# Performance work log

Measured on AMD Instinct MI355X. Metric: run time of the kernel, lower is better.

Reference implementation:

```python
import jax, jax.numpy as jnp
import numpy as np

EPS = 1e-6
DN = ('NCHW', 'OIHW', 'NCHW')


def _dw_conv(s, w, dilation, k):
    pad = dilation * (k - 1) // 2
    return jax.lax.conv_general_dilated(
        s, w, window_strides=(1, 1), padding=[(pad, pad), (pad, pad)],
        rhs_dilation=(dilation, dilation), dimension_numbers=DN,
        feature_group_count=4)


def _branch(s, dw_w, pw_w, pw_b, dilation, k):
    h = _dw_conv(s, dw_w, dilation, k)           # [B,4,H,W]
    # pointwise 1x1 conv 4 -> 1
    return jnp.einsum('bchw,oc->bohw', h, pw_w) + pw_b[None, :, None, None]


def setup_inputs() -> dict:
    key = jax.random.key(0)
    ks = jax.random.split(key, 12)
    B, C, H, W = 32, 64, 128, 128
    nb, rh = 3, 8
    d = {}
    d['x'] = jax.random.normal(ks[0], (B, C, H, W), dtype=jnp.float32)
    # branch 0: k=3 d=1; branch 1: k=7 d=1; branch 2: k=7 d=2
    d['dw0'] = jax.random.normal(ks[1], (4, 1, 3, 3), dtype=jnp.float32) * 0.2
    d['dw1'] = jax.random.normal(ks[2], (4, 1, 7, 7), dtype=jnp.float32) * 0.1
    d['dw2'] = jax.random.normal(ks[3], (4, 1, 7, 7), dtype=jnp.float32) * 0.1
    d['pw0_w'] = jax.random.normal(ks[4], (1, 4), dtype=jnp.float32) * 0.5
    d['pw0_b'] = jnp.zeros((1,), dtype=jnp.float32)
    d['pw1_w'] = jax.random.normal(ks[5], (1, 4), dtype=jnp.float32) * 0.5
    d['pw1_b'] = jnp.zeros((1,), dtype=jnp.float32)
    d['pw2_w'] = jax.random.normal(ks[6], (1, 4), dtype=jnp.float32) * 0.5
    d['pw2_b'] = jnp.zeros((1,), dtype=jnp.float32)
    # router: 1x1 convs on pooled [B,4,1,1] == dense layers
    d['rw1'] = jax.random.normal(ks[7], (rh, 4), dtype=jnp.float32) * 0.5
    d['rb1'] = jnp.zeros((rh,), dtype=jnp.float32)
    d['rw2'] = jax.random.normal(ks[8], (nb, rh), dtype=jnp.float32) * 0.3
    d['rb2'] = jnp.zeros((nb,), dtype=jnp.float32)
    # t_raw = softplus_inverse(1.0)
    d['t_raw'] = jnp.asarray(np.log(np.expm1(1.0)), dtype=jnp.float32)
    return d


def reference(x, dw0, dw1, dw2, pw0_w, pw0_b, pw1_w, pw1_b, pw2_w, pw2_b,
              rw1, rb1, rw2, rb2, t_raw):
    B, C, H, W = x.shape
    avg_map = jnp.mean(x, axis=1, keepdims=True)        # [B,1,H,W]
    max_map = jnp.max(x, axis=1, keepdims=True)         # [B,1,H,W]
    xs = jnp.linspace(-1.0, 1.0, W, dtype=x.dtype)
    ys = jnp.linspace(-1.0, 1.0, H, dtype=x.dtype)
    yy, xx = jnp.meshgrid(ys, xs, indexing='ij')
    xg = jnp.broadcast_to(xx[None, None], (B, 1, H, W))
    yg = jnp.broadcast_to(yy[None, None], (B, 1, H, W))
    s = jnp.concatenate([avg_map, max_map, xg, yg], axis=1)  # [B,4,H,W]

    # router: global avg pool -> 1x1 conv -> relu -> 1x1 conv -> softmax
    pooled = jnp.mean(s, axis=(2, 3))                    # [B,4]
    hid = jax.nn.relu(pooled @ rw1.T + rb1)              # [B,rh]
    logits = hid @ rw2.T + rb2                           # [B,nb]
    rw = jax.nn.softmax(logits, axis=1)                  # [B,nb]

    z = jnp.stack([
        _branch(s, dw0, pw0_w, pw0_b, 1, 3),
        _branch(s, dw1, pw1_w, pw1_b, 1, 7),
        _branch(s, dw2, pw2_w, pw2_b, 2, 7),
    ], axis=1)                                           # [B,nb,1,H,W]

    wlogits = jnp.sum(rw[:, :, None, None, None] * z, axis=1)  # [B,1,H,W]
    T = jax.nn.softplus(t_raw) + EPS
    sa = jax.nn.sigmoid(wlogits / T)                     # [B,1,H,W]
    Y = x * sa                                           # [B,C,H,W]
    return (Y, sa)
```

## Files before the change

kernel.cpp:

```cpp
#include <hip/hip_runtime.h>

#define B_ 32
#define C_ 64
#define H_ 128
#define W_ 128
#define HW_ (H_*W_)
#define CHW_ (C_*HW_)

__global__ __launch_bounds__(256) void k1_reduce(
    const float* __restrict__ x, float* __restrict__ avgmap,
    float* __restrict__ maxmap, float* __restrict__ partial)
{
    int t = blockIdx.x * 256 + threadIdx.x;
    int base = t * 4;
    int b = base >> 14;
    int q = base & (HW_ - 1);
    const float4* xp = (const float4*)(x + (size_t)b * CHW_ + q);
    float4 v = xp[0];
    float4 s = v, m = v;
    #pragma unroll 8
    for (int c = 1; c < C_; ++c) {
        float4 u = xp[c * (HW_ / 4)];
        s.x += u.x; s.y += u.y; s.z += u.z; s.w += u.w;
        m.x = fmaxf(m.x, u.x); m.y = fmaxf(m.y, u.y);
        m.z = fmaxf(m.z, u.z); m.w = fmaxf(m.w, u.w);
    }
    const float inv = 1.0f / C_;
    float4 a = make_float4(s.x * inv, s.y * inv, s.z * inv, s.w * inv);
    ((float4*)avgmap)[t] = a;
    ((float4*)maxmap)[t] = m;

    float la = a.x + a.y + a.z + a.w;
    float lm = m.x + m.y + m.z + m.w;
    #pragma unroll
    for (int o = 32; o > 0; o >>= 1) {
        la += __shfl_down(la, o);
        lm += __shfl_down(lm, o);
    }
    __shared__ float wa[4], wm[4];
    int lane = threadIdx.x & 63, wid = threadIdx.x >> 6;
    if (lane == 0) { wa[wid] = la; wm[wid] = lm; }
    __syncthreads();
    if (threadIdx.x == 0) {
        partial[2 * blockIdx.x]     = wa[0] + wa[1] + wa[2] + wa[3];
        partial[2 * blockIdx.x + 1] = wm[0] + wm[1] + wm[2] + wm[3];
    }
}

__global__ void k2_router(const float* __restrict__ partial,
                          const float* __restrict__ rw1, const float* __restrict__ rb1,
                          const float* __restrict__ rw2, const float* __restrict__ rb2,
                          float* __restrict__ rwout)
{
    int b = threadIdx.x;
    if (b >= B_) return;
    float s0 = 0.0f, s1 = 0.0f;
    #pragma unroll
    for (int i = 0; i < 16; ++i) {
        s0 += partial[2 * (b * 16 + i)];
        s1 += partial[2 * (b * 16 + i) + 1];
    }
    float p0 = s0 * (1.0f / HW_);
    float p1 = s1 * (1.0f / HW_);
    float hid[8];
    #pragma unroll
    for (int j = 0; j < 8; ++j)
        hid[j] = fmaxf(0.0f, rb1[j] + rw1[j * 4] * p0 + rw1[j * 4 + 1] * p1);
    float lg[3];
    #pragma unroll
    for (int i = 0; i < 3; ++i) {
        float acc = rb2[i];
        #pragma unroll
        for (int j = 0; j < 8; ++j) acc += hid[j] * rw2[i * 8 + j];
        lg[i] = acc;
    }
    float mx = fmaxf(lg[0], fmaxf(lg[1], lg[2]));
    float e0 = expf(lg[0] - mx), e1 = expf(lg[1] - mx), e2 = expf(lg[2] - mx);
    float inv = 1.0f / (e0 + e1 + e2);
    rwout[b * 3 + 0] = e0 * inv;
    rwout[b * 3 + 1] = e1 * inv;
    rwout[b * 3 + 2] = e2 * inv;
}

__global__ __launch_bounds__(256) void k34_branches_apply(
    const float* __restrict__ x,
    const float* __restrict__ avgmap, const float* __restrict__ maxmap,
    const float* __restrict__ dw0, const float* __restrict__ dw1,
    const float* __restrict__ dw2,
    const float* __restrict__ pw0w, const float* __restrict__ pw0b,
    const float* __restrict__ pw1w, const float* __restrict__ pw1b,
    const float* __restrict__ pw2w, const float* __restrict__ pw2b,
    const float* __restrict__ rw, const float* __restrict__ t_raw,
    float* __restrict__ y, float* __restrict__ sa_out)
{
    __shared__ float sA[14][140];
    __shared__ float sM[14][140];
    __shared__ float wf0[36], wf1[196], wf2[196];
    __shared__ float ssa[256];

    int b  = blockIdx.y;
    int y0 = blockIdx.x * 2;
    int tix = threadIdx.x;
    const float* am = avgmap + (size_t)b * HW_;
    const float* mm = maxmap + (size_t)b * HW_;

    for (int idx = tix; idx < 14 * 32; idx += 256) {
        int r = idx >> 5, c4 = idx & 31;
        int gy = y0 - 6 + r;
        bool ok = (unsigned)gy < H_;
        float4 av = ok ? ((const float4*)(am + gy * W_))[c4]
                       : make_float4(0.f, 0.f, 0.f, 0.f);
        float4 mv = ok ? ((const float4*)(mm + gy * W_))[c4]
                       : make_float4(0.f, 0.f, 0.f, 0.f);
        float* pa = &sA[r][6 + c4 * 4];
        float* pm = &sM[r][6 + c4 * 4];
        pa[0] = av.x; pa[1] = av.y; pa[2] = av.z; pa[3] = av.w;
        pm[0] = mv.x; pm[1] = mv.y; pm[2] = mv.z; pm[3] = mv.w;
    }
    for (int idx = tix; idx < 14 * 12; idx += 256) {
        int r = idx / 12, c = idx % 12;
        int cc = (c < 6) ? c : (134 + c - 6);
        sA[r][cc] = 0.0f;
        sM[r][cc] = 0.0f;
    }
    if (tix < 36)  wf0[tix] = pw0w[tix / 9]  * dw0[tix];
    if (tix < 196) {
        wf1[tix] = pw1w[tix / 49] * dw1[tix];
        wf2[tix] = pw2w[tix / 49] * dw2[tix];
    }
    __syncthreads();

    int ly = tix >> 7;
    int lx = tix & 127;
    int gy = y0 + ly;
    const float sc = 2.0f / 127.0f;
    const float xv_c = lx * sc - 1.0f;

    float z0 = pw0b[0], z1 = pw1b[0], z2 = pw2b[0];

    #pragma unroll
    for (int ky = 0; ky < 3; ++ky) {
        #pragma unroll
        for (int kx = 0; kx < 3; ++kx) {
            int i = ky - 1, j = kx - 1;
            float a = sA[ly + 6 + i][lx + 6 + j];
            float m = sM[ly + 6 + i][lx + 6 + j];
            int iy = gy + i, ix = lx + j;
            bool ok = ((unsigned)iy < H_) && ((unsigned)ix < W_);
            float xv = ok ? (ix * sc - 1.0f) : 0.0f;
            float yv = ok ? (iy * sc - 1.0f) : 0.0f;
            int t = ky * 3 + kx;
            z0 += wf0[t] * a + wf0[9 + t] * m + wf0[18 + t] * xv + wf0[27 + t] * yv;
        }
    }
    #pragma unroll
    for (int ky = 0; ky < 7; ++ky) {
        #pragma unroll
        for (int kx = 0; kx < 7; ++kx) {
            int i = ky - 3, j = kx - 3;
            float a = sA[ly + 6 + i][lx + 6 + j];
            float m = sM[ly + 6 + i][lx + 6 + j];
            int iy = gy + i, ix = lx + j;
            bool ok = ((unsigned)iy < H_) && ((unsigned)ix < W_);
            float xv = ok ? (ix * sc - 1.0f) : 0.0f;
            float yv = ok ? (iy * sc - 1.0f) : 0.0f;
            int t = ky * 7 + kx;
            z1 += wf1[t] * a + wf1[49 + t] * m + wf1[98 + t] * xv + wf1[147 + t] * yv;
        }
    }
    #pragma unroll
    for (int ky = 0; ky < 7; ++ky) {
        #pragma unroll
        for (int kx = 0; kx < 7; ++kx) {
            int i = (ky - 3) * 2, j = (kx - 3) * 2;
            float a = sA[ly + 6 + i][lx + 6 + j];
            float m = sM[ly + 6 + i][lx + 6 + j];
            int iy = gy + i, ix = lx + j;
            bool ok = ((unsigned)iy < H_) && ((unsigned)ix < W_);
            float xv = ok ? (ix * sc - 1.0f) : 0.0f;
            float yv = ok ? (iy * sc - 1.0f) : 0.0f;
            int t = ky * 7 + kx;
            z2 += wf2[t] * a + wf2[49 + t] * m + wf2[98 + t] * xv + wf2[147 + t] * yv;
        }
    }

    float wl = rw[b * 3] * z0 + rw[b * 3 + 1] * z1 + rw[b * 3 + 2] * z2;
    float T = log1pf(expf(t_raw[0])) + 1e-6f;
    float s = 1.0f / (1.0f + expf(-wl / T));
    ssa[tix] = s;
    sa_out[(size_t)b * HW_ + gy * W_ + lx] = s;
    __syncthreads();

    int wid  = tix >> 6;
    int lane = tix & 63;
    float4 sv = ((const float4*)ssa)[lane];
    const float* xt = x + (size_t)b * CHW_ + y0 * W_;
    float*       yt = y + (size_t)b * CHW_ + y0 * W_;
    #pragma unroll 4
    for (int k = 0; k < 16; ++k) {
        int c = wid + k * 4;
        float4 xv4 = ((const float4*)(xt + c * HW_))[lane];
        float4 yv4 = make_float4(xv4.x * sv.x, xv4.y * sv.y,
                                 xv4.z * sv.z, xv4.w * sv.w);
        ((float4*)(yt + c * HW_))[lane] = yv4;
    }
}

extern "C" void kernel_launch(void* const* d_in, const int* in_sizes, int n_in,
                              void* d_out, int out_size, void* d_ws, size_t ws_size,
                              hipStream_t stream)
{
    const float* x     = (const float*)d_in[0];
    const float* dw0   = (const float*)d_in[1];
    const float* dw1   = (const float*)d_in[2];
    const float* dw2   = (const float*)d_in[3];
    const float* pw0w  = (const float*)d_in[4];
    const float* pw0b  = (const float*)d_in[5];
    const float* pw1w  = (const float*)d_in[6];
    const float* pw1b  = (const float*)d_in[7];
    const float* pw2w  = (const float*)d_in[8];
    const float* pw2b  = (const float*)d_in[9];
    const float* rw1   = (const float*)d_in[10];
    const float* rb1   = (const float*)d_in[11];
    const float* rw2   = (const float*)d_in[12];
    const float* rb2   = (const float*)d_in[13];
    const float* t_raw = (const float*)d_in[14];

    float* ws      = (float*)d_ws;
    float* avgmap  = ws;
    float* maxmap  = ws + 524288;
    float* partial = ws + 1048576;
    float* rw      = ws + 1049600;

    float* Y  = (float*)d_out;
    float* sa = Y + (size_t)B_ * CHW_;

    k1_reduce<<<B_ * HW_ / 4 / 256, 256, 0, stream>>>(x, avgmap, maxmap, partial);
    k2_router<<<1, 64, 0, stream>>>(partial, rw1, rb1, rw2, rb2, rw);

    dim3 g34(H_ / 2, B_);
    k34_branches_apply<<<g34, 256, 0, stream>>>(
        x, avgmap, maxmap, dw0, dw1, dw2,
        pw0w, pw0b, pw1w, pw1b, pw2w, pw2b,
        rw, t_raw, Y, sa);
}
```

Before: 307.4 us.

## Precompute batch-independent coordinate-channel conv terms and enlarge branch tiles

Moves the coordinate-grid contributions of all three depthwise branches, which do not depend on the batch, into a separate small kernel that writes a per-pixel bias map. The main kernel then reads that map, so its convolution loops only process the avg and max channels, and the 3x3 branch reuses the 7x7 row loads. The temperature reciprocal is computed once in the router kernel. Blocks now cover 4 rows with 512 threads, which adds an extra launch and a 3xHW buffer read in exchange for roughly halving the stencil arithmetic.

```diff
diff --git a/kernel.cpp b/kernel.cpp
--- a/kernel.cpp
+++ b/kernel.cpp
@@ -6,6 +6,60 @@
 #define W_ 128
 #define HW_ (H_*W_)
 #define CHW_ (C_*HW_)
+
+__global__ __launch_bounds__(256) void k0_zpos(
+    const float* __restrict__ dw0, const float* __restrict__ dw1,
+    const float* __restrict__ dw2,
+    const float* __restrict__ pw0w, const float* __restrict__ pw0b,
+    const float* __restrict__ pw1w, const float* __restrict__ pw1b,
+    const float* __restrict__ pw2w, const float* __restrict__ pw2b,
+    float* __restrict__ zpos)
+{
+    int p = blockIdx.x * 256 + threadIdx.x;
+    int gy = p >> 7, gx = p & 127;
+    const float sc = 2.0f / 127.0f;
+    float z0 = pw0b[0], z1 = pw1b[0], z2 = pw2b[0];
+    float px0 = pw0w[2], py0 = pw0w[3];
+    float px1 = pw1w[2], py1 = pw1w[3];
+    float px2 = pw2w[2], py2 = pw2w[3];
+
+    #pragma unroll
+    for (int ky = 0; ky < 3; ++ky)
+    #pragma unroll
+    for (int kx = 0; kx < 3; ++kx) {
+        int iy = gy + ky - 1, ix = gx + kx - 1;
+        bool ok = ((unsigned)iy < H_) && ((unsigned)ix < W_);
+        float xv = ok ? ix * sc - 1.0f : 0.0f;
+        float yv = ok ? iy * sc - 1.0f : 0.0f;
+        int t = ky * 3 + kx;
+        z0 += px0 * dw0[18 + t] * xv + py0 * dw0[27 + t] * yv;
+    }
+    #pragma unroll
+    for (int ky = 0; ky < 7; ++ky)
+    #pragma unroll
+    for (int kx = 0; kx < 7; ++kx) {
+        int iy = gy + ky - 3, ix = gx + kx - 3;
+        bool ok = ((unsigned)iy < H_) && ((unsigned)ix < W_);
+        float xv = ok ? ix * sc - 1.0f : 0.0f;
+        float yv = ok ? iy * sc - 1.0f : 0.0f;
+        int t = ky * 7 + kx;
+        z1 += px1 * dw1[98 + t] * xv + py1 * dw1[147 + t] * yv;
+    }
+    #pragma unroll
+    for (int ky = 0; ky < 7; ++ky)
+    #pragma unroll
+    for (int kx = 0; kx < 7; ++kx) {
+        int iy = gy + (ky - 3) * 2, ix = gx + (kx - 3) * 2;
+        bool ok = ((unsigned)iy < H_) && ((unsigned)ix < W_);
+        float xv = ok ? ix * sc - 1.0f : 0.0f;
+        float yv = ok ? iy * sc - 1.0f : 0.0f;
+        int t = ky * 7 + kx;
+        z2 += px2 * dw2[98 + t] * xv + py2 * dw2[147 + t] * yv;
+    }
+    zpos[p]           = z0;
+    zpos[HW_ + p]     = z1;
+    zpos[2 * HW_ + p] = z2;
+}
 
 __global__ __launch_bounds__(256) void k1_reduce(
     const float* __restrict__ x, float* __restrict__ avgmap,
@@ -50,10 +104,13 @@
 __global__ void k2_router(const float* __restrict__ partial,
                           const float* __restrict__ rw1, const float* __restrict__ rb1,
                           const float* __restrict__ rw2, const float* __restrict__ rb2,
+                          const float* __restrict__ t_raw,
                           float* __restrict__ rwout)
 {
     int b = threadIdx.x;
     if (b >= B_) return;
+    if (b == 0)
+        rwout[96] = 1.0f / (log1pf(expf(t_raw[0])) + 1e-6f);
     float s0 = 0.0f, s1 = 0.0f;
     #pragma unroll
     for (int i = 0; i < 16; ++i) {
@@ -82,30 +139,30 @@
     rwout[b * 3 + 2] = e2 * inv;
 }
 
-__global__ __launch_bounds__(256) void k34_branches_apply(
+__global__ __launch_bounds__(512) void k34_branches_apply(
     const float* __restrict__ x,
     const float* __restrict__ avgmap, const float* __restrict__ maxmap,
     const float* __restrict__ dw0, const float* __restrict__ dw1,
     const float* __restrict__ dw2,
-    const float* __restrict__ pw0w, const float* __restrict__ pw0b,
-    const float* __restrict__ pw1w, const float* __restrict__ pw1b,
-    const float* __restrict__ pw2w, const float* __restrict__ pw2b,
-    const float* __restrict__ rw, const float* __restrict__ t_raw,
+    const float* __restrict__ pw0w, const float* __restrict__ pw1w,
+    const float* __restrict__ pw2w,
+    const float* __restrict__ zpos, const float* __restrict__ rw,
     float* __restrict__ y, float* __restrict__ sa_out)
 {
-    __shared__ float sA[14][140];
-    __shared__ float sM[14][140];
-    __shared__ float wf0[36], wf1[196], wf2[196];
-    __shared__ float ssa[256];
+    __shared__ float sA[16][140];
+    __shared__ float sM[16][140];
+    __shared__ float wA0[9], wM0[9];
+    __shared__ float wA1[49], wM1[49], wA2[49], wM2[49];
+    __shared__ __align__(16) float ssa[512];
 
     int b  = blockIdx.y;
-    int y0 = blockIdx.x * 2;
+    int y0 = blockIdx.x * 4;
     int tix = threadIdx.x;
     const float* am = avgmap + (size_t)b * HW_;
     const float* mm = maxmap + (size_t)b * HW_;
 
-    for (int idx = tix; idx < 14 * 32; idx += 256) {
-        int r = idx >> 5, c4 = idx & 31;
+    {
+        int r = tix >> 5, c4 = tix & 31;
         int gy = y0 - 6 + r;
         bool ok = (unsigned)gy < H_;
         float4 av = ok ? ((const float4*)(am + gy * W_))[c4]
@@ -117,92 +174,83 @@
         pa[0] = av.x; pa[1] = av.y; pa[2] = av.z; pa[3] = av.w;
         pm[0] = mv.x; pm[1] = mv.y; pm[2] = mv.z; pm[3] = mv.w;
     }
-    for (int idx = tix; idx < 14 * 12; idx += 256) {
-        int r = idx / 12, c = idx % 12;
+    if (tix < 16 * 12) {
+        int r = tix / 12, c = tix % 12;
         int cc = (c < 6) ? c : (134 + c - 6);
         sA[r][cc] = 0.0f;
         sM[r][cc] = 0.0f;
     }
-    if (tix < 36)  wf0[tix] = pw0w[tix / 9]  * dw0[tix];
-    if (tix < 196) {
-        wf1[tix] = pw1w[tix / 49] * dw1[tix];
-        wf2[tix] = pw2w[tix / 49] * dw2[tix];
-    }
+    if (tix < 9)  { wA0[tix] = pw0w[0] * dw0[tix];
+                    wM0[tix] = pw0w[1] * dw0[9 + tix]; }
+    if (tix < 49) { wA1[tix] = pw1w[0] * dw1[tix];
+                    wM1[tix] = pw1w[1] * dw1[49 + tix];
+                    wA2[tix] = pw2w[0] * dw2[tix];
+                    wM2[tix] = pw2w[1] * dw2[49 + tix]; }
     __syncthreads();
 
     int ly = tix >> 7;
     int lx = tix & 127;
     int gy = y0 + ly;
-    const float sc = 2.0f / 127.0f;
-    const float xv_c = lx * sc - 1.0f;
-
-    float z0 = pw0b[0], z1 = pw1b[0], z2 = pw2b[0];
-
-    #pragma unroll
-    for (int ky = 0; ky < 3; ++ky) {
-        #pragma unroll
-        for (int kx = 0; kx < 3; ++kx) {
-            int i = ky - 1, j = kx - 1;
-            float a = sA[ly + 6 + i][lx + 6 + j];
-            float m = sM[ly + 6 + i][lx + 6 + j];
-            int iy = gy + i, ix = lx + j;
-            bool ok = ((unsigned)iy < H_) && ((unsigned)ix < W_);
-            float xv = ok ? (ix * sc - 1.0f) : 0.0f;
-            float yv = ok ? (iy * sc - 1.0f) : 0.0f;
-            int t = ky * 3 + kx;
-            z0 += wf0[t] * a + wf0[9 + t] * m + wf0[18 + t] * xv + wf0[27 + t] * yv;
+    int pidx = gy * W_ + lx;
+
+    float z0 = zpos[pidx];
+    float z1 = zpos[HW_ + pidx];
+    float z2 = zpos[2 * HW_ + pidx];
+
+    #pragma unroll
+    for (int ky = 0; ky < 7; ++ky) {
+        const float* ra = &sA[ly + 3 + ky][lx + 3];
+        const float* rm = &sM[ly + 3 + ky][lx + 3];
+        float av[7], mv[7];
+        #pragma unroll
+        for (int j = 0; j < 7; ++j) { av[j] = ra[j]; mv[j] = rm[j]; }
+        #pragma unroll
+        for (int j = 0; j < 7; ++j) {
+            int t = ky * 7 + j;
+            z1 += wA1[t] * av[j] + wM1[t] * mv[j];
         }
+        if (ky >= 2 && ky <= 4) {
+            #pragma unroll
+            for (int j = 2; j <= 4; ++j) {
+                int t = (ky - 2) * 3 + (j - 2);
+                z0 += wA0[t] * av[j] + wM0[t] * mv[j];
+            }
+        }
     }
     #pragma unroll
     for (int ky = 0; ky < 7; ++ky) {
+        const float* ra = &sA[ly + 2 * ky][lx];
+        const float* rm = &sM[ly + 2 * ky][lx];
         #pragma unroll
         for (int kx = 0; kx < 7; ++kx) {
-            int i = ky - 3, j = kx - 3;
-            float a = sA[ly + 6 + i][lx + 6 + j];
-            float m = sM[ly + 6 + i][lx + 6 + j];
-            int iy = gy + i, ix = lx + j;
-            bool ok = ((unsigned)iy < H_) && ((unsigned)ix < W_);
-            float xv = ok ? (ix * sc - 1.0f) : 0.0f;
-            float yv = ok ? (iy * sc - 1.0f) : 0.0f;
             int t = ky * 7 + kx;
-            z1 += wf1[t] * a + wf1[49 + t] * m + wf1[98 + t] * xv + wf1[147 + t] * yv;
+            z2 += wA2[t] * ra[2 * kx] + wM2[t] * rm[2 * kx];
         }
     }
-    #pragma unroll
-    for (int ky = 0; ky < 7; ++ky) {
-        #pragma unroll
-        for (int kx = 0; kx < 7; ++kx) {
-            int i = (ky - 3) * 2, j = (kx - 3) * 2;
-            float a = sA[ly + 6 + i][lx + 6 + j];
-            float m = sM[ly + 6 + i][lx + 6 + j];
-            int iy = gy + i, ix = lx + j;
-            bool ok = ((unsigned)iy < H_) && ((unsigned)ix < W_);
-            float xv = ok ? (ix * sc - 1.0f) : 0.0f;
-            float yv = ok ? (iy * sc - 1.0f) : 0.0f;
-            int t = ky * 7 + kx;
-            z2 += wf2[t] * a + wf2[49 + t] * m + wf2[98 + t] * xv + wf2[147 + t] * yv;
-        }
-    }
 
     float wl = rw[b * 3] * z0 + rw[b * 3 + 1] * z1 + rw[b * 3 + 2] * z2;
-    float T = log1pf(expf(t_raw[0])) + 1e-6f;
-    float s = 1.0f / (1.0f + expf(-wl / T));
+    float s = 1.0f / (1.0f + expf(-wl * rw[96]));
     ssa[tix] = s;
-    sa_out[(size_t)b * HW_ + gy * W_ + lx] = s;
+    sa_out[(size_t)b * HW_ + pidx] = s;
     __syncthreads();
 
     int wid  = tix >> 6;
     int lane = tix & 63;
-    float4 sv = ((const float4*)ssa)[lane];
+    float4 sv0 = ((const float4*)ssa)[lane];
+    float4 sv1 = ((const float4*)ssa)[64 + lane];
     const float* xt = x + (size_t)b * CHW_ + y0 * W_;
     float*       yt = y + (size_t)b * CHW_ + y0 * W_;
     #pragma unroll 4
-    for (int k = 0; k < 16; ++k) {
-        int c = wid + k * 4;
-        float4 xv4 = ((const float4*)(xt + c * HW_))[lane];
-        float4 yv4 = make_float4(xv4.x * sv.x, xv4.y * sv.y,
-                                 xv4.z * sv.z, xv4.w * sv.w);
-        ((float4*)(yt + c * HW_))[lane] = yv4;
+    for (int k = 0; k < 8; ++k) {
+        int c = wid + k * 8;
+        const float4* xp = (const float4*)(xt + c * HW_);
+        float4*       yp = (float4*)(yt + c * HW_);
+        float4 a0 = xp[lane];
+        float4 a1 = xp[64 + lane];
+        yp[lane]      = make_float4(a0.x * sv0.x, a0.y * sv0.y,
+                                    a0.z * sv0.z, a0.w * sv0.w);
+        yp[64 + lane] = make_float4(a1.x * sv1.x, a1.y * sv1.y,
+                                    a1.z * sv1.z, a1.w * sv1.w);
     }
 }
 
@@ -231,16 +279,18 @@
     float* maxmap  = ws + 524288;
     float* partial = ws + 1048576;
     float* rw      = ws + 1049600;
+    float* zpos    = ws + 1049728;
 
     float* Y  = (float*)d_out;
     float* sa = Y + (size_t)B_ * CHW_;
 
+    k0_zpos<<<HW_ / 256, 256, 0, stream>>>(
+        dw0, dw1, dw2, pw0w, pw0b, pw1w, pw1b, pw2w, pw2b, zpos);
     k1_reduce<<<B_ * HW_ / 4 / 256, 256, 0, stream>>>(x, avgmap, maxmap, partial);
-    k2_router<<<1, 64, 0, stream>>>(partial, rw1, rb1, rw2, rb2, rw);
-
-    dim3 g34(H_ / 2, B_);
-    k34_branches_apply<<<g34, 256, 0, stream>>>(
+    k2_router<<<1, 64, 0, stream>>>(partial, rw1, rb1, rw2, rb2, t_raw, rw);
+
+    dim3 g34(H_ / 4, B_);
+    k34_branches_apply<<<g34, 512, 0, stream>>>(
         x, avgmap, maxmap, dw0, dw1, dw2,
-        pw0w, pw0b, pw1w, pw1b, pw2w, pw2b,
-        rw, t_raw, Y, sa);
-}
+        pw0w, pw1w, pw2w, zpos, rw, Y, sa);
+}
```

New measurement: 334.4 us. +8.8%, slower.
